# Kernel tuning notes

Measured on AMD Instinct MI355X. Metric: run time of the kernel, lower is better.

Reference implementation:

```python
import jax, jax.numpy as jnp
import numpy as np

N_NODES = 40000
N_EDGES = 640000
D_IN = 128
D_OUT = 128


def setup_inputs() -> dict:
    key = jax.random.key(0)
    k_feat, k_src, k_dst, k_ws, k_wn = jax.random.split(key, 5)
    feat = jax.random.normal(k_feat, (N_NODES, D_IN), dtype=jnp.float32)
    src = jax.random.randint(k_src, (N_EDGES,), 0, N_NODES, dtype=jnp.int32)
    dst = jax.random.randint(k_dst, (N_EDGES,), 0, N_NODES, dtype=jnp.int32)
    # Glorot-ish init for the two dense layers
    scale = 1.0 / np.sqrt(D_IN)
    W_self = jax.random.normal(k_ws, (D_IN, D_OUT), dtype=jnp.float32) * scale
    W_neigh = jax.random.normal(k_wn, (D_IN, D_OUT), dtype=jnp.float32) * scale
    b_self = jnp.zeros((D_OUT,), dtype=jnp.float32)
    b_neigh = jnp.zeros((D_OUT,), dtype=jnp.float32)
    return {"feat": feat, "src": src, "dst": dst,
            "W_self": W_self, "b_self": b_self,
            "W_neigh": W_neigh, "b_neigh": b_neigh}


def reference(feat, src, dst, W_self, b_self, W_neigh, b_neigh):
    # --- mean aggregation: copy_src('h','m') + mean('m','neigh') ---
    # Gather source features along edges, segment-sum into dst, divide by in-degree.
    msgs = feat[src]  # [E, D_in]
    neigh_sum = jax.ops.segment_sum(msgs, dst, num_segments=N_NODES)  # [N, D_in]
    deg = jax.ops.segment_sum(jnp.ones((src.shape[0],), feat.dtype), dst,
                              num_segments=N_NODES)  # [N]
    # DGL mean reducer yields 0 for nodes with no incoming edges.
    h_neigh = neigh_sum / jnp.maximum(deg, 1.0)[:, None]
    # --- fc_self(h_self) + fc_neigh(h_neigh) ---
    rst = (feat @ W_self + b_self) + (h_neigh @ W_neigh + b_neigh)
    return rst
```

## Files before the change

kernel.cpp:

```cpp
#include <hip/hip_runtime.h>
#include <cstddef>

constexpr int NN  = 40000;
constexpr int NE  = 640000;
constexpr int DIM = 128;
constexpr int CAP = 48;
constexpr int PLANE = NN * 64;

typedef __attribute__((ext_vector_type(8))) short short8;
typedef __attribute__((ext_vector_type(4))) float floatx4;

__device__ __forceinline__ unsigned short f2bf(float x) {
    union { float f; unsigned int i; } v; v.f = x;
    unsigned int u = v.i;
    return (unsigned short)((u + 0x7fffu + ((u >> 16) & 1u)) >> 16);
}
__device__ __forceinline__ float bflo2f(unsigned int u) {
    union { unsigned int i; float f; } v; v.i = u << 16; return v.f;
}
__device__ __forceinline__ float bfhi2f(unsigned int u) {
    union { unsigned int i; float f; } v; v.i = u & 0xffff0000u; return v.f;
}

__global__ __launch_bounds__(256) void k_prep(
    const float* __restrict__ feat, const float* __restrict__ Wself,
    const float* __restrict__ Wneigh, unsigned short* __restrict__ featb,
    unsigned short* __restrict__ Wc, int* __restrict__ cnt)
{
    int b = blockIdx.x, t = threadIdx.x;
    if (b < 2500) {
        int idx8 = b * 256 + t;
        int n  = idx8 >> 4;
        int d0 = (idx8 & 15) << 3;
        const float4* fp =
            reinterpret_cast<const float4*>(feat + (size_t)n * DIM + d0);
        float4 v0 = fp[0], v1 = fp[1];
        unsigned int p0 = (unsigned int)f2bf(v0.x) | ((unsigned int)f2bf(v0.y) << 16);
        unsigned int p1 = (unsigned int)f2bf(v0.z) | ((unsigned int)f2bf(v0.w) << 16);
        unsigned int p2 = (unsigned int)f2bf(v1.x) | ((unsigned int)f2bf(v1.y) << 16);
        unsigned int p3 = (unsigned int)f2bf(v1.z) | ((unsigned int)f2bf(v1.w) << 16);
        int plane = d0 >> 6, off = d0 & 63;
        *reinterpret_cast<uint4*>(
            featb + (size_t)plane * PLANE + (size_t)n * 64 + off) =
            make_uint4(p0, p1, p2, p3);
    } else if (b < 2628) {
        int idx = (b - 2500) * 256 + t;
        int c = idx >> 13, n = (idx >> 6) & 127, kp = idx & 63;
        int k = c * 64 + kp;
        float w = (k < DIM) ? Wself[(size_t)k * DIM + n]
                            : Wneigh[(size_t)(k - DIM) * DIM + n];
        Wc[idx] = f2bf(w);
    } else {
        int i = (b - 2628) * 256 + t;
        if (i < NN) cnt[i] = 0;
    }
}

__global__ __launch_bounds__(256) void k_fill(
    const int* __restrict__ src, const int* __restrict__ dst,
    int* __restrict__ cnt, unsigned short* __restrict__ colf)
{
    int e = blockIdx.x * blockDim.x + threadIdx.x;
    if (e < NE) {
        int d = dst[e];
        int pos = atomicAdd(&cnt[d], 1);
        if (pos < CAP) colf[d * CAP + pos] = (unsigned short)src[e];
    }
}

__global__ __launch_bounds__(256) void k_gather(
    const unsigned int* __restrict__ fb32,
    const int* __restrict__ cnt,
    const unsigned short* __restrict__ colf,
    unsigned int* __restrict__ hnb32)
{
    int gtid = blockIdx.x * blockDim.x + threadIdx.x;
    int n = gtid >> 6;
    if (n >= NN) return;
    int lane = threadIdx.x & 63;

    int deg = cnt[n];
    int m = min(deg, CAP);
    int sv = (lane < m) ? (int)colf[n * CAP + lane] : 0;

    int vb = (lane >> 5) * (NN * 32) + (lane & 31);
    float ax0 = 0.f, ay0 = 0.f, ax1 = 0.f, ay1 = 0.f;
    int i = 0;
    for (; i + 3 < m; i += 4) {
        int s0 = __shfl(sv, i),     s1 = __shfl(sv, i + 1);
        int s2 = __shfl(sv, i + 2), s3 = __shfl(sv, i + 3);
        unsigned int u0 = fb32[vb + s0 * 32];
        unsigned int u1 = fb32[vb + s1 * 32];
        unsigned int u2 = fb32[vb + s2 * 32];
        unsigned int u3 = fb32[vb + s3 * 32];
        ax0 += bflo2f(u0); ay0 += bfhi2f(u0);
        ax1 += bflo2f(u1); ay1 += bfhi2f(u1);
        ax0 += bflo2f(u2); ay0 += bfhi2f(u2);
        ax1 += bflo2f(u3); ay1 += bfhi2f(u3);
    }
    for (; i < m; ++i) {
        int s0 = __shfl(sv, i);
        unsigned int u0 = fb32[vb + s0 * 32];
        ax0 += bflo2f(u0); ay0 += bfhi2f(u0);
    }
    float inv = 1.0f / fmaxf((float)deg, 1.0f);
    float ax = (ax0 + ax1) * inv, ay = (ay0 + ay1) * inv;
    hnb32[vb + n * 32] = (unsigned int)f2bf(ax) | ((unsigned int)f2bf(ay) << 16);
}

__global__ __launch_bounds__(320) void k_gemm(
    const unsigned short* __restrict__ featb,
    const unsigned short* __restrict__ hnb,
    const unsigned short* __restrict__ Wc,
    const float* __restrict__ bself, const float* __restrict__ bneigh,
    float* __restrict__ out)
{
    __shared__ unsigned short As[160 * 64];
    __shared__ unsigned short Bs[128 * 64];

    int t = threadIdx.x;
    int w = t >> 6;
    int lane = t & 63;
    int base_m = blockIdx.x * 160;

    floatx4 acc[2][8];
    #pragma unroll
    for (int a = 0; a < 2; ++a)
        #pragma unroll
        for (int b = 0; b < 8; ++b) acc[a][b] = (floatx4)0.f;

    for (int c = 0; c < 4; ++c) {
        const unsigned short* srcp =
            ((c < 2) ? featb + (size_t)c * PLANE
                     : hnb + (size_t)(c - 2) * PLANE) + (size_t)base_m * 64;
        #pragma unroll
        for (int it = 0; it < 4; ++it) {
            int slot = t + it * 320;
            __builtin_amdgcn_global_load_lds(
                (const __attribute__((address_space(1))) unsigned int*)(srcp + slot * 8),
                (__attribute__((address_space(3))) unsigned int*)(As + slot * 8),
                16, 0, 0);
        }
        if (t < 256) {
            const unsigned short* bp = Wc + (size_t)c * 128 * 64;
            #pragma unroll
            for (int it = 0; it < 4; ++it) {
                int slot = t + it * 256;
                __builtin_amdgcn_global_load_lds(
                    (const __attribute__((address_space(1))) unsigned int*)(bp + slot * 8),
                    (__attribute__((address_space(3))) unsigned int*)(Bs + slot * 8),
                    16, 0, 0);
            }
        }
        __syncthreads();

        #pragma unroll
        for (int s = 0; s < 2; ++s) {
            int koff = s * 32 + (lane >> 4) * 8;
            short8 af[2];
            #pragma unroll
            for (int mt = 0; mt < 2; ++mt) {
                int m = w * 32 + mt * 16 + (lane & 15);
                af[mt] = *reinterpret_cast<const short8*>(As + m * 64 + koff);
            }
            #pragma unroll
            for (int nt = 0; nt < 8; ++nt) {
                int n = nt * 16 + (lane & 15);
                short8 bf = *reinterpret_cast<const short8*>(Bs + n * 64 + koff);
                acc[0][nt] = __builtin_amdgcn_mfma_f32_16x16x32_bf16(
                    af[0], bf, acc[0][nt], 0, 0, 0);
                acc[1][nt] = __builtin_amdgcn_mfma_f32_16x16x32_bf16(
                    af[1], bf, acc[1][nt], 0, 0, 0);
            }
        }
        __syncthreads();
    }

    int colb = lane & 15;
    int quad = lane >> 4;
    #pragma unroll
    for (int nt = 0; nt < 8; ++nt) {
        int col = nt * 16 + colb;
        float bb = bself[col] + bneigh[col];
        #pragma unroll
        for (int mt = 0; mt < 2; ++mt) {
            #pragma unroll
            for (int r = 0; r < 4; ++r) {
                int row = base_m + w * 32 + mt * 16 + quad * 4 + r;
                out[(size_t)row * DIM + col] = acc[mt][nt][r] + bb;
            }
        }
    }
}

extern "C" void kernel_launch(void* const* d_in, const int* in_sizes, int n_in,
                              void* d_out, int out_size, void* d_ws, size_t ws_size,
                              hipStream_t stream)
{
    const float* feat   = (const float*)d_in[0];
    const int*   src    = (const int*)d_in[1];
    const int*   dst    = (const int*)d_in[2];
    const float* Wself  = (const float*)d_in[3];
    const float* bself  = (const float*)d_in[4];
    const float* Wneigh = (const float*)d_in[5];
    const float* bneigh = (const float*)d_in[6];
    float* out = (float*)d_out;

    char* ws = (char*)d_ws;
    unsigned short* featb = (unsigned short*)(ws);
    unsigned short* hnb   = (unsigned short*)(ws + 10240000);
    unsigned short* colf  = (unsigned short*)(ws + 20480000);
    unsigned short* Wc    = (unsigned short*)(ws + 24320000);
    int*            cnt   = (int*)(ws + 24385536);

    k_prep<<<2785, 256, 0, stream>>>(feat, Wself, Wneigh, featb, Wc, cnt);

    k_fill<<<(NE + 255) / 256, 256, 0, stream>>>(src, dst, cnt, colf);

    k_gather<<<(NN * 64) / 256, 256, 0, stream>>>(
        (const unsigned int*)featb, cnt, colf, (unsigned int*)hnb);

    k_gemm<<<NN / 160, 320, 0, stream>>>(featb, hnb, Wc, bself, bneigh, out);
}
```

Measured before the change: 147.8 us.

## Load GEMM operands directly from global memory and widen gather unroll to 8

```diff
diff --git a/kernel.cpp b/kernel.cpp
--- a/kernel.cpp
+++ b/kernel.cpp
@@ -84,27 +84,28 @@
     int sv = (lane < m) ? (int)colf[n * CAP + lane] : 0;
 
     int vb = (lane >> 5) * (NN * 32) + (lane & 31);
-    float ax0 = 0.f, ay0 = 0.f, ax1 = 0.f, ay1 = 0.f;
+    float a0 = 0.f, b0 = 0.f, a1 = 0.f, b1 = 0.f;
     int i = 0;
-    for (; i + 3 < m; i += 4) {
-        int s0 = __shfl(sv, i),     s1 = __shfl(sv, i + 1);
-        int s2 = __shfl(sv, i + 2), s3 = __shfl(sv, i + 3);
-        unsigned int u0 = fb32[vb + s0 * 32];
-        unsigned int u1 = fb32[vb + s1 * 32];
-        unsigned int u2 = fb32[vb + s2 * 32];
-        unsigned int u3 = fb32[vb + s3 * 32];
-        ax0 += bflo2f(u0); ay0 += bfhi2f(u0);
-        ax1 += bflo2f(u1); ay1 += bfhi2f(u1);
-        ax0 += bflo2f(u2); ay0 += bfhi2f(u2);
-        ax1 += bflo2f(u3); ay1 += bfhi2f(u3);
+    for (; i + 7 < m; i += 8) {
+        unsigned int u[8];
+        #pragma unroll
+        for (int q = 0; q < 8; ++q) {
+            int s = __shfl(sv, i + q);
+            u[q] = fb32[vb + s * 32];
+        }
+        #pragma unroll
+        for (int q = 0; q < 8; q += 2) {
+            a0 += bflo2f(u[q]);     b0 += bfhi2f(u[q]);
+            a1 += bflo2f(u[q + 1]); b1 += bfhi2f(u[q + 1]);
+        }
     }
     for (; i < m; ++i) {
-        int s0 = __shfl(sv, i);
-        unsigned int u0 = fb32[vb + s0 * 32];
-        ax0 += bflo2f(u0); ay0 += bfhi2f(u0);
+        int s = __shfl(sv, i);
+        unsigned int u0 = fb32[vb + s * 32];
+        a0 += bflo2f(u0); b0 += bfhi2f(u0);
     }
     float inv = 1.0f / fmaxf((float)deg, 1.0f);
-    float ax = (ax0 + ax1) * inv, ay = (ay0 + ay1) * inv;
+    float ax = (a0 + a1) * inv, ay = (b0 + b1) * inv;
     hnb32[vb + n * 32] = (unsigned int)f2bf(ax) | ((unsigned int)f2bf(ay) << 16);
 }
 
@@ -115,13 +116,14 @@
     const float* __restrict__ bself, const float* __restrict__ bneigh,
     float* __restrict__ out)
 {
-    __shared__ unsigned short As[160 * 64];
-    __shared__ unsigned short Bs[128 * 64];
-
     int t = threadIdx.x;
     int w = t >> 6;
     int lane = t & 63;
-    int base_m = blockIdx.x * 160;
+    int colb = lane & 15;
+    int quad = lane >> 4;
+    int base_m = blockIdx.x * 160 + w * 32;
+    int mrow = base_m + colb;
+    int koff = quad * 8;
 
     floatx4 acc[2][8];
     #pragma unroll
@@ -129,55 +131,35 @@
         #pragma unroll
         for (int b = 0; b < 8; ++b) acc[a][b] = (floatx4)0.f;
 
+    const unsigned short* Ap0 = featb;
+    const unsigned short* Ap1 = featb + PLANE;
+    const unsigned short* Ap2 = hnb;
+    const unsigned short* Ap3 = hnb + PLANE;
+    const unsigned short* planes[4] = {Ap0, Ap1, Ap2, Ap3};
+
+    #pragma unroll
     for (int c = 0; c < 4; ++c) {
-        const unsigned short* srcp =
-            ((c < 2) ? featb + (size_t)c * PLANE
-                     : hnb + (size_t)(c - 2) * PLANE) + (size_t)base_m * 64;
-        #pragma unroll
-        for (int it = 0; it < 4; ++it) {
-            int slot = t + it * 320;
-            __builtin_amdgcn_global_load_lds(
-                (const __attribute__((address_space(1))) unsigned int*)(srcp + slot * 8),
-                (__attribute__((address_space(3))) unsigned int*)(As + slot * 8),
-                16, 0, 0);
-        }
-        if (t < 256) {
-            const unsigned short* bp = Wc + (size_t)c * 128 * 64;
-            #pragma unroll
-            for (int it = 0; it < 4; ++it) {
-                int slot = t + it * 256;
-                __builtin_amdgcn_global_load_lds(
-                    (const __attribute__((address_space(1))) unsigned int*)(bp + slot * 8),
-                    (__attribute__((address_space(3))) unsigned int*)(Bs + slot * 8),
-                    16, 0, 0);
-            }
-        }
-        __syncthreads();
-
+        const unsigned short* Ap = planes[c];
+        const unsigned short* Bp = Wc + c * (128 * 64);
         #pragma unroll
         for (int s = 0; s < 2; ++s) {
-            int koff = s * 32 + (lane >> 4) * 8;
-            short8 af[2];
-            #pragma unroll
-            for (int mt = 0; mt < 2; ++mt) {
-                int m = w * 32 + mt * 16 + (lane & 15);
-                af[mt] = *reinterpret_cast<const short8*>(As + m * 64 + koff);
-            }
+            int kk = s * 32 + koff;
+            short8 a0 = *reinterpret_cast<const short8*>(
+                Ap + (size_t)mrow * 64 + kk);
+            short8 a1 = *reinterpret_cast<const short8*>(
+                Ap + (size_t)(mrow + 16) * 64 + kk);
             #pragma unroll
             for (int nt = 0; nt < 8; ++nt) {
-                int n = nt * 16 + (lane & 15);
-                short8 bf = *reinterpret_cast<const short8*>(Bs + n * 64 + koff);
+                int n = nt * 16 + colb;
+                short8 bf = *reinterpret_cast<const short8*>(Bp + n * 64 + kk);
                 acc[0][nt] = __builtin_amdgcn_mfma_f32_16x16x32_bf16(
-                    af[0], bf, acc[0][nt], 0, 0, 0);
+                    a0, bf, acc[0][nt], 0, 0, 0);
                 acc[1][nt] = __builtin_amdgcn_mfma_f32_16x16x32_bf16(
-                    af[1], bf, acc[1][nt], 0, 0, 0);
+                    a1, bf, acc[1][nt], 0, 0, 0);
             }
         }
-        __syncthreads();
-    }
-
-    int colb = lane & 15;
-    int quad = lane >> 4;
+    }
+
     #pragma unroll
     for (int nt = 0; nt < 8; ++nt) {
         int col = nt * 16 + colb;
@@ -186,7 +168,7 @@
         for (int mt = 0; mt < 2; ++mt) {
             #pragma unroll
             for (int r = 0; r < 4; ++r) {
-                int row = base_m + w * 32 + mt * 16 + quad * 4 + r;
+                int row = base_m + mt * 16 + quad * 4 + r;
                 out[(size_t)row * DIM + col] = acc[mt][nt][r] + bb;
             }
         }
```

After: 156.0 us. 1.06x slower.
